# Kernel tuning notes

Measured on AMD Instinct MI355X. Metric: run time of the kernel, lower is better.

Reference implementation:

```python
import jax, jax.numpy as jnp
import numpy as np

FP16_HUGE = 2.0 ** 15
NUM_HEAD = 4
LN_EPS = 1e-5


def setup_inputs() -> dict:
    key = jax.random.key(0)
    ks = jax.random.split(key, 12)
    B, N, D = 1, 256, 128
    H = NUM_HEAD
    inp = {
        "pair_act": jax.random.normal(ks[0], (B, N, N, D), dtype=jnp.float32),
        "pair_mask": jnp.ones((B, N, N), dtype=jnp.float32),
        "ln_scale": jnp.ones((D,), dtype=jnp.float32),
        "ln_bias": jnp.zeros((D,), dtype=jnp.float32),
        # torch Linear weight layout: [out_dim, in_dim]; applied as x @ W.T
        "w2d": jax.random.normal(ks[1], (H, D), dtype=jnp.float32) / np.sqrt(D),
        "wq": jax.random.normal(ks[2], (D, D), dtype=jnp.float32) / np.sqrt(D),
        "wk": jax.random.normal(ks[3], (D, D), dtype=jnp.float32) / np.sqrt(D),
        "wv": jax.random.normal(ks[4], (D, D), dtype=jnp.float32) / np.sqrt(D),
        "wg": jax.random.normal(ks[5], (D, D), dtype=jnp.float32) / np.sqrt(D),
        "bg": jnp.ones((D,), dtype=jnp.float32),  # gating bias init = 1.0
        "wo": jax.random.normal(ks[6], (D, D), dtype=jnp.float32) * 0.02,
        "bo": jnp.zeros((D,), dtype=jnp.float32),
    }
    return inp


def reference(pair_act, pair_mask, ln_scale, ln_bias, w2d, wq, wk, wv, wg, bg, wo, bo):
    B, N, _, D = pair_act.shape
    H = NUM_HEAD
    kd = D // H  # per-head key/value dim
    scale = kd ** (-0.5)

    # mask bias: [B, N(row), 1, 1, N(key)]
    bias = (FP16_HUGE * (pair_mask - 1.0))[:, :, None, None, :]

    # LayerNorm (fp32, eps=1e-5)
    mu = jnp.mean(pair_act, axis=-1, keepdims=True)
    var = jnp.mean(jnp.square(pair_act - mu), axis=-1, keepdims=True)
    x = (pair_act - mu) * jax.lax.rsqrt(var + LN_EPS) * ln_scale + ln_bias

    # non-batched per-head bias: [B, 1, H, N, N]
    nb = jnp.einsum("bijd,hd->bhij", x, w2d)[:, None]

    q = (x @ wq.T).reshape(B, N, N, H, kd) * scale  # [B, r, i, H, kd]
    k = (x @ wk.T).reshape(B, N, N, H, kd)
    v = (x @ wv.T).reshape(B, N, N, H, kd)

    logits = jnp.einsum("brihk,brjhk->brhij", q, k) + bias + nb  # [B, r, H, i, j]
    w = jax.nn.softmax(logits, axis=-1)
    o = jnp.einsum("brhij,brjhv->brihv", w, v)  # [B, r, i, H, kd]

    g = jax.nn.sigmoid(x @ wg.T + bg).reshape(B, N, N, H, kd)
    o = (o * g).reshape(B, N, N, D)

    out = o @ wo.T + bo
    return out * pair_mask[..., None]
```

## Files before the change

### kernel.cpp

```cpp
#include <hip/hip_runtime.h>
#include <hip/hip_bf16.h>

typedef unsigned short u16;
typedef __attribute__((ext_vector_type(8))) short bf16x8;
typedef __attribute__((ext_vector_type(4))) float f32x4;

#define N 256
#define D 128
#define NH 4
#define KD 32
#define NN 65536
#define QK_SCALE 0.17677669529663687f
#define HUGE_MASK 32768.0f

__device__ __forceinline__ float b2f(u16 s) {
  union { float f; unsigned u; } x; x.u = ((unsigned)s) << 16; return x.f;
}
__device__ __forceinline__ u16 f2b(float f) {
  union { float f; unsigned u; } x; x.f = f;
  unsigned r = x.u + 0x7fff + ((x.u >> 16) & 1);
  return (u16)(r >> 16);
}

__device__ __forceinline__ void stage_w(const float* __restrict__ W, u16* Wlds, int tid) {
  int row = tid >> 1, cb = (tid & 1) * 64;
#pragma unroll
  for (int j = 0; j < 8; j++) {
    float4 f0 = *(const float4*)(W + row * 128 + cb + j * 8);
    float4 f1 = *(const float4*)(W + row * 128 + cb + j * 8 + 4);
    uint4 pk;
    pk.x = (unsigned)f2b(f0.x) | ((unsigned)f2b(f0.y) << 16);
    pk.y = (unsigned)f2b(f0.z) | ((unsigned)f2b(f0.w) << 16);
    pk.z = (unsigned)f2b(f1.x) | ((unsigned)f2b(f1.y) << 16);
    pk.w = (unsigned)f2b(f1.z) | ((unsigned)f2b(f1.w) << 16);
    int g = (cb >> 3) + j;
    int gp = (g + (row & 15)) & 15;
    *(uint4*)(&Wlds[row * 128 + gp * 8]) = pk;
  }
}

__global__ __launch_bounds__(256) void projln_kernel(
    const float* __restrict__ pa, const float* __restrict__ lns, const float* __restrict__ lnb,
    const float* __restrict__ w2d,
    const float* __restrict__ wq, const float* __restrict__ wk,
    const float* __restrict__ wv, const float* __restrict__ wg,
    const float* __restrict__ bg,
    u16* __restrict__ q, u16* __restrict__ k, u16* __restrict__ v, u16* __restrict__ g,
    float* __restrict__ nb)
{
  __shared__ __align__(16) u16 Wlds[128 * 128];
  int tid = threadIdx.x;
  int wave = tid >> 6, lane = tid & 63;
  int lr = lane & 15, quad = lane >> 4;

  bf16x8 a[2][4];
#pragma unroll
  for (int mt = 0; mt < 2; mt++) {
    int row = blockIdx.x * 128 + wave * 32 + mt * 16 + lr;
    const float* rp = pa + (size_t)row * D;
    float xv[4][8];
    float s = 0.f, ss = 0.f;
#pragma unroll
    for (int ks = 0; ks < 4; ks++) {
      float4 a0 = *(const float4*)(rp + ks * 32 + quad * 8);
      float4 a1 = *(const float4*)(rp + ks * 32 + quad * 8 + 4);
      xv[ks][0] = a0.x; xv[ks][1] = a0.y; xv[ks][2] = a0.z; xv[ks][3] = a0.w;
      xv[ks][4] = a1.x; xv[ks][5] = a1.y; xv[ks][6] = a1.z; xv[ks][7] = a1.w;
#pragma unroll
      for (int j = 0; j < 8; j++) { s += xv[ks][j]; ss += xv[ks][j] * xv[ks][j]; }
    }
    s  += __shfl_xor(s, 16, 64);  ss += __shfl_xor(ss, 16, 64);
    s  += __shfl_xor(s, 32, 64);  ss += __shfl_xor(ss, 32, 64);
    float mu = s * (1.0f / D);
    float var = ss * (1.0f / D) - mu * mu;
    float rs = rsqrtf(var + 1e-5f);
#pragma unroll
    for (int ks = 0; ks < 4; ks++) {
      float4 s0 = *(const float4*)(lns + ks * 32 + quad * 8);
      float4 s1 = *(const float4*)(lns + ks * 32 + quad * 8 + 4);
      float4 b0 = *(const float4*)(lnb + ks * 32 + quad * 8);
      float4 b1 = *(const float4*)(lnb + ks * 32 + quad * 8 + 4);
      float sc[8] = {s0.x,s0.y,s0.z,s0.w,s1.x,s1.y,s1.z,s1.w};
      float bi[8] = {b0.x,b0.y,b0.z,b0.w,b1.x,b1.y,b1.z,b1.w};
#pragma unroll
      for (int j = 0; j < 8; j++) xv[ks][j] = (xv[ks][j] - mu) * rs * sc[j] + bi[j];
    }
#pragma unroll
    for (int h = 0; h < NH; h++) {
      float p = 0.f;
#pragma unroll
      for (int ks = 0; ks < 4; ks++) {
        float4 w0 = *(const float4*)(w2d + h * D + ks * 32 + quad * 8);
        float4 w1 = *(const float4*)(w2d + h * D + ks * 32 + quad * 8 + 4);
        p += xv[ks][0]*w0.x + xv[ks][1]*w0.y + xv[ks][2]*w0.z + xv[ks][3]*w0.w
           + xv[ks][4]*w1.x + xv[ks][5]*w1.y + xv[ks][6]*w1.z + xv[ks][7]*w1.w;
      }
      p += __shfl_xor(p, 16, 64);
      p += __shfl_xor(p, 32, 64);
      if (quad == 0) nb[(size_t)h * NN + row] = p;
    }
#pragma unroll
    for (int ks = 0; ks < 4; ks++)
#pragma unroll
      for (int j = 0; j < 8; j++) a[mt][ks][j] = (short)f2b(xv[ks][j]);
  }

  const float* Ws[4] = {wq, wk, wv, wg};
  u16* Os[4] = {q, k, v, g};
#pragma unroll
  for (int mat = 0; mat < 4; mat++) {
    stage_w(Ws[mat], Wlds, tid);
    __syncthreads();
    f32x4 acc[2][2][4];
#pragma unroll
    for (int mt = 0; mt < 2; mt++)
#pragma unroll
      for (int tg = 0; tg < 2; tg++)
#pragma unroll
        for (int e = 0; e < 4; e++) acc[mt][tg][e] = (f32x4){0.f, 0.f, 0.f, 0.f};
#pragma unroll
    for (int ks = 0; ks < 4; ks++) {
#pragma unroll
      for (int tg = 0; tg < 2; tg++) {
#pragma unroll
        for (int e = 0; e < 4; e++) {
          int nrow = tg * 64 + 4 * lr + e;
          int gp = (ks * 4 + quad + (nrow & 15)) & 15;
          bf16x8 b = *(const bf16x8*)(&Wlds[nrow * 128 + gp * 8]);
          acc[0][tg][e] = __builtin_amdgcn_mfma_f32_16x16x32_bf16(a[0][ks], b, acc[0][tg][e], 0, 0, 0);
          acc[1][tg][e] = __builtin_amdgcn_mfma_f32_16x16x32_bf16(a[1][ks], b, acc[1][tg][e], 0, 0, 0);
        }
      }
    }
    u16* O = Os[mat];
#pragma unroll
    for (int mt = 0; mt < 2; mt++) {
      int row0 = blockIdx.x * 128 + wave * 32 + mt * 16 + quad * 4;
#pragma unroll
      for (int tg = 0; tg < 2; tg++) {
        int c0 = tg * 64 + 4 * lr;
        float bg0 = 0.f, bg1 = 0.f, bg2 = 0.f, bg3 = 0.f;
        if (mat == 3) { bg0 = bg[c0]; bg1 = bg[c0+1]; bg2 = bg[c0+2]; bg3 = bg[c0+3]; }
#pragma unroll
        for (int reg = 0; reg < 4; reg++) {
          float v0 = acc[mt][tg][0][reg], v1 = acc[mt][tg][1][reg];
          float v2 = acc[mt][tg][2][reg], v3 = acc[mt][tg][3][reg];
          if (mat == 0) { v0 *= QK_SCALE; v1 *= QK_SCALE; v2 *= QK_SCALE; v3 *= QK_SCALE; }
          if (mat == 3) {
            v0 = 1.0f / (1.0f + __expf(-(v0 + bg0)));
            v1 = 1.0f / (1.0f + __expf(-(v1 + bg1)));
            v2 = 1.0f / (1.0f + __expf(-(v2 + bg2)));
            v3 = 1.0f / (1.0f + __expf(-(v3 + bg3)));
          }
          uint2 pk;
          pk.x = (unsigned)f2b(v0) | ((unsigned)f2b(v1) << 16);
          pk.y = (unsigned)f2b(v2) | ((unsigned)f2b(v3) << 16);
          *(uint2*)(O + (size_t)(row0 + reg) * D + c0) = pk;
        }
      }
    }
    __syncthreads();
  }
}

#define KSTRIDE 40
#define VSTRIDE 264
#define PSTRIDE 264
__global__ __launch_bounds__(256) void attn_kernel(
    const u16* __restrict__ q, const u16* __restrict__ k, const u16* __restrict__ v,
    const u16* __restrict__ g, const float* __restrict__ nb, const float* __restrict__ mask,
    u16* __restrict__ og)
{
  __shared__ __align__(16) u16 Kt[256 * KSTRIDE];
  __shared__ __align__(16) u16 Vt[32 * VSTRIDE];
  __shared__ __align__(16) u16 P[4 * 16 * PSTRIDE];
  int h = blockIdx.x & 3, r = blockIdx.x >> 2;
  int tid = threadIdx.x;
  {
    const u16* krow = k + ((size_t)r * N + tid) * D + h * KD;
#pragma unroll
    for (int ii = 0; ii < 4; ii++)
      *(bf16x8*)(&Kt[tid * KSTRIDE + ii * 8]) = *(const bf16x8*)(krow + ii * 8);
    const u16* vrow = v + ((size_t)r * N + tid) * D + h * KD;
#pragma unroll
    for (int c = 0; c < KD; c++)
      Vt[c * VSTRIDE + tid] = vrow[c];
  }
  __syncthreads();
  int wave = tid >> 6, lane = tid & 63;
  int lr = lane & 15, quad = lane >> 4;
  u16* Pw = &P[wave * 16 * PSTRIDE];

  for (int pass = 0; pass < 4; pass++) {
    int i0 = pass * 64 + wave * 16;
    bf16x8 af = *(const bf16x8*)(q + ((size_t)r * N + i0 + lr) * D + h * KD + quad * 8);
    f32x4 S[16];
#pragma unroll
    for (int t = 0; t < 16; t++) {
      bf16x8 bfr = *(const bf16x8*)(&Kt[(t * 16 + lr) * KSTRIDE + quad * 8]);
      S[t] = __builtin_amdgcn_mfma_f32_16x16x32_bf16(af, bfr, (f32x4){0.f,0.f,0.f,0.f}, 0, 0, 0);
    }
    float mx[4] = {-3e38f, -3e38f, -3e38f, -3e38f};
#pragma unroll
    for (int t = 0; t < 16; t++) {
      int j = t * 16 + lr;
      float bias = HUGE_MASK * (mask[r * N + j] - 1.0f);
      const float* nbp = &nb[(size_t)h * NN + (size_t)(i0 + quad * 4) * N + j];
#pragma unroll
      for (int reg = 0; reg < 4; reg++) {
        float val = S[t][reg] + bias + nbp[(size_t)reg * N];
        S[t][reg] = val;
        mx[reg] = fmaxf(mx[reg], val);
      }
    }
#pragma unroll
    for (int reg = 0; reg < 4; reg++) {
#pragma unroll
      for (int off = 8; off; off >>= 1)
        mx[reg] = fmaxf(mx[reg], __shfl_xor(mx[reg], off, 16));
    }
    float lsum[4] = {0.f, 0.f, 0.f, 0.f};
#pragma unroll
    for (int t = 0; t < 16; t++) {
#pragma unroll
      for (int reg = 0; reg < 4; reg++) {
        float p = __expf(S[t][reg] - mx[reg]);
        S[t][reg] = p;
        lsum[reg] += p;
      }
    }
#pragma unroll
    for (int reg = 0; reg < 4; reg++) {
#pragma unroll
      for (int off = 8; off; off >>= 1)
        lsum[reg] += __shfl_xor(lsum[reg], off, 16);
    }
#pragma unroll
    for (int t = 0; t < 16; t++) {
#pragma unroll
      for (int reg = 0; reg < 4; reg++)
        Pw[(quad * 4 + reg) * PSTRIDE + t * 16 + lr] = f2b(S[t][reg]);
    }
    __syncthreads();
    f32x4 o[2] = {(f32x4){0.f,0.f,0.f,0.f}, (f32x4){0.f,0.f,0.f,0.f}};
#pragma unroll
    for (int ks = 0; ks < 8; ks++) {
      bf16x8 pa = *(const bf16x8*)(&Pw[lr * PSTRIDE + ks * 32 + quad * 8]);
#pragma unroll
      for (int u = 0; u < 2; u++) {
        bf16x8 vb = *(const bf16x8*)(&Vt[(u * 16 + lr) * VSTRIDE + ks * 32 + quad * 8]);
        o[u] = __builtin_amdgcn_mfma_f32_16x16x32_bf16(pa, vb, o[u], 0, 0, 0);
      }
    }
#pragma unroll
    for (int u = 0; u < 2; u++) {
#pragma unroll
      for (int reg = 0; reg < 4; reg++) {
        int i = i0 + quad * 4 + reg;
        int c = h * KD + u * 16 + lr;
        size_t idx = ((size_t)r * N + i) * D + c;
        float val = o[u][reg] / lsum[reg] * b2f(g[idx]);
        og[idx] = f2b(val);
      }
    }
  }
}

__global__ __launch_bounds__(256) void out_kernel(
    const u16* __restrict__ og, const float* __restrict__ wo, const float* __restrict__ bo,
    const float* __restrict__ mask, float* __restrict__ out)
{
  __shared__ __align__(16) u16 Wlds[128 * 128];
  int tid = threadIdx.x;
  stage_w(wo, Wlds, tid);
  int wave = tid >> 6, lane = tid & 63;
  int lr = lane & 15, quad = lane >> 4;
  bf16x8 a[2][4];
#pragma unroll
  for (int mt = 0; mt < 2; mt++) {
    int arow = blockIdx.x * 128 + wave * 32 + mt * 16 + lr;
#pragma unroll
    for (int ks = 0; ks < 4; ks++)
      a[mt][ks] = *(const bf16x8*)(og + (size_t)arow * D + ks * 32 + quad * 8);
  }
  __syncthreads();
  f32x4 acc[2][2][4];
#pragma unroll
  for (int mt = 0; mt < 2; mt++)
#pragma unroll
    for (int tg = 0; tg < 2; tg++)
#pragma unroll
      for (int e = 0; e < 4; e++) acc[mt][tg][e] = (f32x4){0.f, 0.f, 0.f, 0.f};
#pragma unroll
  for (int ks = 0; ks < 4; ks++) {
#pragma unroll
    for (int tg = 0; tg < 2; tg++) {
#pragma unroll
      for (int e = 0; e < 4; e++) {
        int nrow = tg * 64 + 4 * lr + e;
        int gp = (ks * 4 + quad + (nrow & 15)) & 15;
        bf16x8 b = *(const bf16x8*)(&Wlds[nrow * 128 + gp * 8]);
        acc[0][tg][e] = __builtin_amdgcn_mfma_f32_16x16x32_bf16(a[0][ks], b, acc[0][tg][e], 0, 0, 0);
        acc[1][tg][e] = __builtin_amdgcn_mfma_f32_16x16x32_bf16(a[1][ks], b, acc[1][tg][e], 0, 0, 0);
      }
    }
  }
#pragma unroll
  for (int mt = 0; mt < 2; mt++) {
    int row0 = blockIdx.x * 128 + wave * 32 + mt * 16 + quad * 4;
#pragma unroll
    for (int tg = 0; tg < 2; tg++) {
      int c0 = tg * 64 + 4 * lr;
      float4 bo4 = *(const float4*)(bo + c0);
#pragma unroll
      for (int reg = 0; reg < 4; reg++) {
        int pos = row0 + reg;
        float m = mask[pos];
        float4 o4;
        o4.x = (acc[mt][tg][0][reg] + bo4.x) * m;
        o4.y = (acc[mt][tg][1][reg] + bo4.y) * m;
        o4.z = (acc[mt][tg][2][reg] + bo4.z) * m;
        o4.w = (acc[mt][tg][3][reg] + bo4.w) * m;
        *(float4*)(out + (size_t)pos * D + c0) = o4;
      }
    }
  }
}

extern "C" void kernel_launch(void* const* d_in, const int* in_sizes, int n_in,
                              void* d_out, int out_size, void* d_ws, size_t ws_size,
                              hipStream_t stream)
{
  const float* pa   = (const float*)d_in[0];
  const float* mask = (const float*)d_in[1];
  const float* lns  = (const float*)d_in[2];
  const float* lnb  = (const float*)d_in[3];
  const float* w2d  = (const float*)d_in[4];
  const float* wq   = (const float*)d_in[5];
  const float* wk   = (const float*)d_in[6];
  const float* wv   = (const float*)d_in[7];
  const float* wg   = (const float*)d_in[8];
  const float* bg   = (const float*)d_in[9];
  const float* wo   = (const float*)d_in[10];
  const float* bo   = (const float*)d_in[11];

  const size_t ARR = (size_t)NN * D;
  u16* q  = (u16*)d_ws;
  u16* k  = q + ARR;
  u16* v  = k + ARR;
  u16* g  = v + ARR;
  u16* og = g + ARR;
  float* nb = (float*)(og + ARR);

  projln_kernel<<<512, 256, 0, stream>>>(pa, lns, lnb, w2d, wq, wk, wv, wg, bg, q, k, v, g, nb);
  attn_kernel<<<N * NH, 256, 0, stream>>>(q, k, v, g, nb, mask, og);
  out_kernel<<<512, 256, 0, stream>>>(og, wo, bo, mask, (float*)d_out);
}
```

Before: 217.2 us.

## Transpose nb bias, use fragment-ordered LDS layouts in attention, drop block barrier

```diff
diff --git a/kernel.cpp b/kernel.cpp
--- a/kernel.cpp
+++ b/kernel.cpp
@@ -46,7 +46,7 @@
     const float* __restrict__ wv, const float* __restrict__ wg,
     const float* __restrict__ bg,
     u16* __restrict__ q, u16* __restrict__ k, u16* __restrict__ v, u16* __restrict__ g,
-    float* __restrict__ nb)
+    float* __restrict__ nbT)
 {
   __shared__ __align__(16) u16 Wlds[128 * 128];
   int tid = threadIdx.x;
@@ -97,7 +97,8 @@
       }
       p += __shfl_xor(p, 16, 64);
       p += __shfl_xor(p, 32, 64);
-      if (quad == 0) nb[(size_t)h * NN + row] = p;
+      if (quad == 0)
+        nbT[(size_t)h * NN + (size_t)(row & 255) * 256 + (row >> 8)] = p;
     }
 #pragma unroll
     for (int ks = 0; ks < 4; ks++)
@@ -163,33 +164,39 @@
   }
 }
 
-#define KSTRIDE 40
-#define VSTRIDE 264
-#define PSTRIDE 264
 __global__ __launch_bounds__(256) void attn_kernel(
     const u16* __restrict__ q, const u16* __restrict__ k, const u16* __restrict__ v,
-    const u16* __restrict__ g, const float* __restrict__ nb, const float* __restrict__ mask,
+    const u16* __restrict__ g, const float* __restrict__ nbT, const float* __restrict__ mask,
     u16* __restrict__ og)
 {
-  __shared__ __align__(16) u16 Kt[256 * KSTRIDE];
-  __shared__ __align__(16) u16 Vt[32 * VSTRIDE];
-  __shared__ __align__(16) u16 P[4 * 16 * PSTRIDE];
+  __shared__ __align__(16) u16 Kf[8192];
+  __shared__ __align__(16) u16 Vf[8192];
+  __shared__ __align__(16) u16 Pf[16384];
+  __shared__ float bias_lds[256];
   int h = blockIdx.x & 3, r = blockIdx.x >> 2;
   int tid = threadIdx.x;
   {
-    const u16* krow = k + ((size_t)r * N + tid) * D + h * KD;
-#pragma unroll
-    for (int ii = 0; ii < 4; ii++)
-      *(bf16x8*)(&Kt[tid * KSTRIDE + ii * 8]) = *(const bf16x8*)(krow + ii * 8);
-    const u16* vrow = v + ((size_t)r * N + tid) * D + h * KD;
-#pragma unroll
-    for (int c = 0; c < KD; c++)
-      Vt[c * VSTRIDE + tid] = vrow[c];
+    int j = tid;
+    const u16* krow = k + ((size_t)r * N + j) * D + h * KD;
+    int t = j >> 4, lrj = j & 15;
+#pragma unroll
+    for (int qc = 0; qc < 4; qc++)
+      *(bf16x8*)(&Kf[((t * 4 + qc) * 16 + lrj) * 8]) = *(const bf16x8*)(krow + qc * 8);
+    const u16* vrow = v + ((size_t)r * N + j) * D + h * KD;
+    int ks = j >> 5, qj = (j >> 3) & 3, jj = j & 7;
+#pragma unroll
+    for (int c = 0; c < 32; c++)
+      Vf[(((ks * 2 + (c & 1)) * 4 + qj) * 16 + (c >> 1)) * 8 + jj] = vrow[c];
+    bias_lds[tid] = HUGE_MASK * (mask[r * N + tid] - 1.0f);
   }
   __syncthreads();
   int wave = tid >> 6, lane = tid & 63;
   int lr = lane & 15, quad = lane >> 4;
-  u16* Pw = &P[wave * 16 * PSTRIDE];
+  u16* Pw = &Pf[wave * 4096];
+  float bias_v[16];
+#pragma unroll
+  for (int t = 0; t < 16; t++) bias_v[t] = bias_lds[t * 16 + lr];
+  const float* nbh = nbT + (size_t)h * NN;
 
   for (int pass = 0; pass < 4; pass++) {
     int i0 = pass * 64 + wave * 16;
@@ -197,36 +204,36 @@
     f32x4 S[16];
 #pragma unroll
     for (int t = 0; t < 16; t++) {
-      bf16x8 bfr = *(const bf16x8*)(&Kt[(t * 16 + lr) * KSTRIDE + quad * 8]);
+      bf16x8 bfr = *(const bf16x8*)(&Kf[((t * 4 + quad) * 16 + lr) * 8]);
       S[t] = __builtin_amdgcn_mfma_f32_16x16x32_bf16(af, bfr, (f32x4){0.f,0.f,0.f,0.f}, 0, 0, 0);
     }
     float mx[4] = {-3e38f, -3e38f, -3e38f, -3e38f};
+#pragma unroll
+    for (int t = 0; t < 16; t++) {
+      float4 nb4 = *(const float4*)(nbh + (size_t)(t * 16 + lr) * N + i0 + quad * 4);
+      float bl = bias_v[t];
+      S[t][0] += nb4.x + bl;  S[t][1] += nb4.y + bl;
+      S[t][2] += nb4.z + bl;  S[t][3] += nb4.w + bl;
+      mx[0] = fmaxf(mx[0], S[t][0]); mx[1] = fmaxf(mx[1], S[t][1]);
+      mx[2] = fmaxf(mx[2], S[t][2]); mx[3] = fmaxf(mx[3], S[t][3]);
+    }
+#pragma unroll
+    for (int reg = 0; reg < 4; reg++) {
+#pragma unroll
+      for (int off = 8; off; off >>= 1)
+        mx[reg] = fmaxf(mx[reg], __shfl_xor(mx[reg], off, 16));
+    }
+    float lsum[4] = {0.f, 0.f, 0.f, 0.f};
 #pragma unroll
     for (int t = 0; t < 16; t++) {
       int j = t * 16 + lr;
-      float bias = HUGE_MASK * (mask[r * N + j] - 1.0f);
-      const float* nbp = &nb[(size_t)h * NN + (size_t)(i0 + quad * 4) * N + j];
-#pragma unroll
-      for (int reg = 0; reg < 4; reg++) {
-        float val = S[t][reg] + bias + nbp[(size_t)reg * N];
-        S[t][reg] = val;
-        mx[reg] = fmaxf(mx[reg], val);
-      }
-    }
-#pragma unroll
-    for (int reg = 0; reg < 4; reg++) {
-#pragma unroll
-      for (int off = 8; off; off >>= 1)
-        mx[reg] = fmaxf(mx[reg], __shfl_xor(mx[reg], off, 16));
-    }
-    float lsum[4] = {0.f, 0.f, 0.f, 0.f};
-#pragma unroll
-    for (int t = 0; t < 16; t++) {
+      int cbase = ((j >> 5) * 4 + ((j >> 3) & 3)) * 128 + (j & 7);
 #pragma unroll
       for (int reg = 0; reg < 4; reg++) {
         float p = __expf(S[t][reg] - mx[reg]);
-        S[t][reg] = p;
         lsum[reg] += p;
+        union { float f; unsigned u; } cv; cv.f = p;
+        Pw[cbase + (quad * 4 + reg) * 8] = (u16)((cv.u + 0x8000u) >> 16);
       }
     }
 #pragma unroll
@@ -235,33 +242,26 @@
       for (int off = 8; off; off >>= 1)
         lsum[reg] += __shfl_xor(lsum[reg], off, 16);
     }
-#pragma unroll
-    for (int t = 0; t < 16; t++) {
-#pragma unroll
-      for (int reg = 0; reg < 4; reg++)
-        Pw[(quad * 4 + reg) * PSTRIDE + t * 16 + lr] = f2b(S[t][reg]);
-    }
-    __syncthreads();
+    __asm__ __volatile__("s_waitcnt lgkmcnt(0)" ::: "memory");
     f32x4 o[2] = {(f32x4){0.f,0.f,0.f,0.f}, (f32x4){0.f,0.f,0.f,0.f}};
 #pragma unroll
     for (int ks = 0; ks < 8; ks++) {
-      bf16x8 pa = *(const bf16x8*)(&Pw[lr * PSTRIDE + ks * 32 + quad * 8]);
-#pragma unroll
-      for (int u = 0; u < 2; u++) {
-        bf16x8 vb = *(const bf16x8*)(&Vt[(u * 16 + lr) * VSTRIDE + ks * 32 + quad * 8]);
-        o[u] = __builtin_amdgcn_mfma_f32_16x16x32_bf16(pa, vb, o[u], 0, 0, 0);
-      }
-    }
-#pragma unroll
-    for (int u = 0; u < 2; u++) {
-#pragma unroll
-      for (int reg = 0; reg < 4; reg++) {
-        int i = i0 + quad * 4 + reg;
-        int c = h * KD + u * 16 + lr;
-        size_t idx = ((size_t)r * N + i) * D + c;
-        float val = o[u][reg] / lsum[reg] * b2f(g[idx]);
-        og[idx] = f2b(val);
-      }
+      bf16x8 pa = *(const bf16x8*)(&Pw[((ks * 4 + quad) * 16 + lr) * 8]);
+#pragma unroll
+      for (int e = 0; e < 2; e++) {
+        bf16x8 vb = *(const bf16x8*)(&Vf[(((ks * 2 + e) * 4 + quad) * 16 + lr) * 8]);
+        o[e] = __builtin_amdgcn_mfma_f32_16x16x32_bf16(pa, vb, o[e], 0, 0, 0);
+      }
+    }
+#pragma unroll
+    for (int reg = 0; reg < 4; reg++) {
+      float inv = __builtin_amdgcn_rcpf(lsum[reg]);
+      int i = i0 + quad * 4 + reg;
+      size_t base = ((size_t)r * N + i) * D + h * KD + 2 * lr;
+      unsigned gv = *(const unsigned*)(g + base);
+      float r0 = o[0][reg] * inv * b2f((u16)(gv & 0xffff));
+      float r1 = o[1][reg] * inv * b2f((u16)(gv >> 16));
+      *(unsigned*)(og + base) = (unsigned)f2b(r0) | ((unsigned)f2b(r1) << 16);
     }
   }
 }
@@ -350,9 +350,9 @@
   u16* v  = k + ARR;
   u16* g  = v + ARR;
   u16* og = g + ARR;
-  float* nb = (float*)(og + ARR);
-
-  projln_kernel<<<512, 256, 0, stream>>>(pa, lns, lnb, w2d, wq, wk, wv, wg, bg, q, k, v, g, nb);
-  attn_kernel<<<N * NH, 256, 0, stream>>>(q, k, v, g, nb, mask, og);
+  float* nbT = (float*)(og + ARR);
+
+  projln_kernel<<<512, 256, 0, stream>>>(pa, lns, lnb, w2d, wq, wk, wv, wg, bg, q, k, v, g, nbT);
+  attn_kernel<<<N * NH, 256, 0, stream>>>(q, k, v, g, nbT, mask, og);
   out_kernel<<<512, 256, 0, stream>>>(og, wo, bo, mask, (float*)d_out);
 }
```

Result: faster. 202.3 us (-6.9%).
